# Kernel optimization log

Hardware: AMD Instinct MI355X
Metric: run time of the kernel (lower is better)

The kernel has to match this reference:

```python
import jax, jax.numpy as jnp
import numpy as np

B, M, D = 2048, 128, 5          # batch, max_atoms, max_degree
F_A, F_B, C = 62, 6, 128        # atom feats, bond feats, conv_width


def setup_inputs() -> dict:
    key = jax.random.key(0)
    k1, k2, k3, k4, k5 = jax.random.split(key, 5)
    atoms = jax.random.normal(k1, (B, M, F_A), dtype=jnp.float32)
    bonds = jax.random.uniform(k2, (B, M, D, F_B), dtype=jnp.float32)
    # edges in [-1, M-1]; -1 = no neighbour (padding)
    edges = jax.random.randint(k3, (B, M, D), 0, M + 1, dtype=jnp.int32) - 1
    fan = F_A + F_B
    scale = float(np.sqrt(2.0 / (fan + C)))
    W_inner = jax.random.normal(k4, (D, fan, C), dtype=jnp.float32) * scale
    b_inner = jnp.zeros((D, C), dtype=jnp.float32)
    W_self = jax.random.normal(k5, (fan, C), dtype=jnp.float32) * scale
    b_self = jnp.zeros((C,), dtype=jnp.float32)
    return {"atoms": atoms, "bonds": bonds, "edges": edges,
            "W_inner": W_inner, "b_inner": b_inner,
            "W_self": W_self, "b_self": b_self}


def reference(atoms, bonds, edges, W_inner, b_inner, W_self, b_self):
    # --- encode() of TiedGraphAutoencoder (encode_only=True) ---
    b = atoms.shape[0]
    # atom degree = number of non-(-1) entries per atom  (B, M)
    deg = jnp.sum((edges != -1).astype(jnp.float32), axis=-1)

    # neighbour_lookup: pad a zero atom at index 0, shift edges by +1,
    # batched gather -> (B, M, D, F_A)
    padded = jnp.pad(atoms, ((0, 0), (1, 0), (0, 0)))
    neigh = padded[jnp.arange(b)[:, None, None], edges + 1]

    summed_atoms = neigh.sum(axis=-2)          # (B, M, F_A)
    summed_bonds = bonds.sum(axis=-2)          # (B, M, F_B)
    summed_features = jnp.concatenate([summed_atoms, summed_bonds], axis=-1)

    # per-degree TimeDistributed Dense + relu, masked by (deg == d), summed
    h = jax.nn.relu(jnp.einsum('bmf,dfc->bmdc', summed_features, W_inner)
                    + b_inner)                 # (B, M, D, C)
    mask = (deg[..., None] == jnp.arange(D, dtype=jnp.float32)).astype(h.dtype)
    zni = jnp.einsum('bmdc,bmd->bmc', h, mask)  # (B, M, C)

    # self connection: dense on [atoms, summed_bonds]
    vxi = jnp.concatenate([atoms, summed_bonds], axis=-1)
    zxi = jax.nn.relu(vxi @ W_self + b_self)    # (B, M, C)

    return zni + zxi
```

## Files before the change

kernel.cpp:

```cpp
#include <hip/hip_runtime.h>

#define NB 2048
#define NM 128
#define ND 5
#define NFA 62
#define NFB 6
#define NFAN 68
#define NC 128
#define LDA 104
#define LDSF 72
#define CHUNK 32

typedef __bf16 bf16x8 __attribute__((ext_vector_type(8)));
typedef float floatx4 __attribute__((ext_vector_type(4)));

__device__ __forceinline__ unsigned short f2bf(float x) {
    unsigned u = __builtin_bit_cast(unsigned, x);
    u += 0x7FFFu + ((u >> 16) & 1u);
    return (unsigned short)(u >> 16);
}

__global__ __launch_bounds__(256) void tga_mfma(
    const float* __restrict__ atoms,
    const float* __restrict__ bonds,
    const int*   __restrict__ edges,
    const float* __restrict__ W_inner,
    const float* __restrict__ b_inner,
    const float* __restrict__ W_self,
    const float* __restrict__ b_self,
    float* __restrict__ out)
{
    __shared__ __align__(16) unsigned short s_A[NM * LDA];
    __shared__ __align__(16) unsigned short s_B[NC * LDA];
    __shared__ __align__(16) float s_sf[CHUNK * LDSF];
    __shared__ int s_list[NM];
    __shared__ int s_nlist;

    const int tid = threadIdx.x;
    const int b   = blockIdx.x;
    if (tid == 0) s_nlist = 0;

    const float* atoms_b = atoms + (size_t)b * (NM * NFA);
    const int*   edges_b = edges + (size_t)b * (NM * ND);
    const float* bonds_b = bonds + (size_t)b * (NM * ND * NFB);
    float*       out_b   = out   + (size_t)b * (NM * NC);

    for (int i = tid; i < NM * 31; i += 256) {
        int m = i / 31, p = i - m * 31;
        float2 v = *(const float2*)&atoms_b[m * NFA + 2 * p];
        unsigned pack = (unsigned)f2bf(v.x) | ((unsigned)f2bf(v.y) << 16);
        *(unsigned*)&s_A[m * LDA + 2 * p] = pack;
    }
    for (int i = tid; i < NM * 7; i += 256) {
        int m = i / 7, q = i - m * 7;
        *(unsigned long long*)&s_A[m * LDA + 68 + 4 * q] = 0ULL;
    }
    for (int i = tid; i < NFAN * NC; i += 256) {
        int f = i >> 7, c2 = i & 127;
        s_B[c2 * LDA + f] = f2bf(W_self[i]);
    }
    for (int i = tid; i < NC * 7; i += 256) {
        int c2 = i / 7, q = i - c2 * 7;
        *(unsigned long long*)&s_B[c2 * LDA + 68 + 4 * q] = 0ULL;
    }

    {
        const int m = tid >> 1, half = tid & 1;
        if (half == 0) {
            const int* e = edges_b + m * ND;
            int deg = 0;
            #pragma unroll
            for (int j = 0; j < ND; ++j) deg += (e[j] >= 0);
            if (deg < ND) {
                int slot = atomicAdd(&s_nlist, 1);
                s_list[slot] = m | (deg << 16);
            }
        } else {
            const float* bp = bonds_b + m * (ND * NFB);
            float sb[NFB] = {0.f, 0.f, 0.f, 0.f, 0.f, 0.f};
            #pragma unroll
            for (int p = 0; p < 15; ++p) {
                float2 v = *(const float2*)&bp[2 * p];
                sb[(2 * p) % NFB]     += v.x;
                sb[(2 * p + 1) % NFB] += v.y;
            }
            *(unsigned*)&s_A[m * LDA + 62] = (unsigned)f2bf(sb[0]) | ((unsigned)f2bf(sb[1]) << 16);
            *(unsigned*)&s_A[m * LDA + 64] = (unsigned)f2bf(sb[2]) | ((unsigned)f2bf(sb[3]) << 16);
            *(unsigned*)&s_A[m * LDA + 66] = (unsigned)f2bf(sb[4]) | ((unsigned)f2bf(sb[5]) << 16);
        }
    }
    __syncthreads();

    {
        const int lane = tid & 63;
        const int wave = tid >> 6;
        const int col  = lane & 15;
        const int quad = lane >> 4;
        const int m0   = wave * 32;

        float bias[8];
        #pragma unroll
        for (int nt = 0; nt < 8; ++nt) bias[nt] = b_self[nt * 16 + col];

        floatx4 acc[16];
        #pragma unroll
        for (int t = 0; t < 16; ++t) {
            floatx4 v; v[0] = v[1] = v[2] = v[3] = bias[t & 7];
            acc[t] = v;
        }

        #pragma unroll
        for (int k = 0; k < 3; ++k) {
            const int koff = k * 32 + quad * 8;
            bf16x8 a0 = *(const bf16x8*)&s_A[(m0 + col) * LDA + koff];
            bf16x8 a1 = *(const bf16x8*)&s_A[(m0 + 16 + col) * LDA + koff];
            #pragma unroll
            for (int nt = 0; nt < 8; ++nt) {
                bf16x8 bf = *(const bf16x8*)&s_B[(nt * 16 + col) * LDA + koff];
                acc[nt]     = __builtin_amdgcn_mfma_f32_16x16x32_bf16(a0, bf, acc[nt],     0, 0, 0);
                acc[8 + nt] = __builtin_amdgcn_mfma_f32_16x16x32_bf16(a1, bf, acc[8 + nt], 0, 0, 0);
            }
        }

        #pragma unroll
        for (int mt = 0; mt < 2; ++mt) {
            #pragma unroll
            for (int nt = 0; nt < 8; ++nt) {
                #pragma unroll
                for (int r = 0; r < 4; ++r) {
                    int m = m0 + mt * 16 + quad * 4 + r;
                    out_b[m * NC + nt * 16 + col] = fmaxf(acc[mt * 8 + nt][r], 0.0f);
                }
            }
        }
    }
    __syncthreads();

    const int nl = s_nlist;
    const int c  = tid & 127;
    const int rg = tid >> 7;

    for (int base = 0; base < nl; base += CHUNK) {
        if (tid < 2 * CHUNK) {
            const int r = tid >> 1, half = tid & 1;
            if (base + r < nl) {
                const int m = s_list[base + r] & 0xFFFF;
                const int* e = edges_b + m * ND;
                int ev[ND];
                #pragma unroll
                for (int j = 0; j < ND; ++j) ev[j] = e[j];

                if (half == 0) {
                    float v[32];
                    #pragma unroll
                    for (int j = 0; j < 32; ++j) v[j] = 0.f;
                    #pragma unroll
                    for (int j = 0; j < ND; ++j) {
                        if (ev[j] >= 0) {
                            const float* ap = atoms_b + ev[j] * NFA;
                            #pragma unroll
                            for (int p = 0; p < 16; ++p) {
                                float2 t = *(const float2*)&ap[2 * p];
                                v[2 * p] += t.x; v[2 * p + 1] += t.y;
                            }
                        }
                    }
                    #pragma unroll
                    for (int q = 0; q < 8; ++q)
                        *(float4*)&s_sf[r * LDSF + 4 * q] = make_float4(v[4*q], v[4*q+1], v[4*q+2], v[4*q+3]);
                } else {
                    float v[36];
                    #pragma unroll
                    for (int j = 0; j < 30; ++j) v[j] = 0.f;
                    #pragma unroll
                    for (int j = 0; j < ND; ++j) {
                        if (ev[j] >= 0) {
                            const float* ap = atoms_b + ev[j] * NFA;
                            #pragma unroll
                            for (int p = 0; p < 15; ++p) {
                                float2 t = *(const float2*)&ap[32 + 2 * p];
                                v[2 * p] += t.x; v[2 * p + 1] += t.y;
                            }
                        }
                    }
                    const float* bp = bonds_b + m * (ND * NFB);
                    float sb[NFB] = {0.f, 0.f, 0.f, 0.f, 0.f, 0.f};
                    #pragma unroll
                    for (int p = 0; p < 15; ++p) {
                        float2 t = *(const float2*)&bp[2 * p];
                        sb[(2 * p) % NFB]     += t.x;
                        sb[(2 * p + 1) % NFB] += t.y;
                    }
                    #pragma unroll
                    for (int j = 0; j < NFB; ++j) v[30 + j] = sb[j];
                    #pragma unroll
                    for (int q = 0; q < 9; ++q)
                        *(float4*)&s_sf[r * LDSF + 32 + 4 * q] = make_float4(v[4*q], v[4*q+1], v[4*q+2], v[4*q+3]);
                }
            }
        }
        __syncthreads();

        const int nrows = min(nl - base, CHUNK);
        for (int r = rg; r < nrows; r += 2) {
            const int packed = s_list[base + r];
            const int m = packed & 0xFFFF;
            const int d = packed >> 16;
            const float* Wd = W_inner + (size_t)d * (NFAN * NC) + c;
            float acc1 = b_inner[d * NC + c];
            #pragma unroll
            for (int q = 0; q < 17; ++q) {
                float4 v = *(const float4*)&s_sf[r * LDSF + 4 * q];
                acc1 += v.x * Wd[(4 * q) * NC] + v.y * Wd[(4 * q + 1) * NC]
                      + v.z * Wd[(4 * q + 2) * NC] + v.w * Wd[(4 * q + 3) * NC];
            }
            out_b[m * NC + c] += fmaxf(acc1, 0.0f);
        }
        __syncthreads();
    }
}

extern "C" void kernel_launch(void* const* d_in, const int* in_sizes, int n_in,
                              void* d_out, int out_size, void* d_ws, size_t ws_size,
                              hipStream_t stream) {
    const float* atoms   = (const float*)d_in[0];
    const float* bonds   = (const float*)d_in[1];
    const int*   edges   = (const int*)d_in[2];
    const float* W_inner = (const float*)d_in[3];
    const float* b_inner = (const float*)d_in[4];
    const float* W_self  = (const float*)d_in[5];
    const float* b_self  = (const float*)d_in[6];
    float* out = (float*)d_out;

    tga_mfma<<<NB, 256, 0, stream>>>(atoms, bonds, edges, W_inner, b_inner,
                                     W_self, b_self, out);
}
```

Before: 268.4 us.

## Pre-convert W_self to bf16 in a prep kernel and read it from global

```diff
diff --git a/kernel.cpp b/kernel.cpp
--- a/kernel.cpp
+++ b/kernel.cpp
@@ -7,9 +7,10 @@
 #define NFB 6
 #define NFAN 68
 #define NC 128
+#define KP 96
 #define LDA 104
 #define LDSF 72
-#define CHUNK 32
+#define CHUNK 16
 
 typedef __bf16 bf16x8 __attribute__((ext_vector_type(8)));
 typedef float floatx4 __attribute__((ext_vector_type(4)));
@@ -20,18 +21,27 @@
     return (unsigned short)(u >> 16);
 }
 
-__global__ __launch_bounds__(256) void tga_mfma(
+__global__ __launch_bounds__(256) void prep_w(const float* __restrict__ W_self,
+                                              unsigned short* __restrict__ wsb) {
+    const int i = blockIdx.x * 256 + threadIdx.x;
+    const int c = i / KP;
+    const int f = i - c * KP;
+    unsigned short v = 0;
+    if (f < NFAN) v = f2bf(W_self[f * NC + c]);
+    wsb[i] = v;
+}
+
+__global__ __launch_bounds__(256, 4) void tga_mfma(
     const float* __restrict__ atoms,
     const float* __restrict__ bonds,
     const int*   __restrict__ edges,
     const float* __restrict__ W_inner,
     const float* __restrict__ b_inner,
-    const float* __restrict__ W_self,
     const float* __restrict__ b_self,
+    const unsigned short* __restrict__ wsb,
     float* __restrict__ out)
 {
     __shared__ __align__(16) unsigned short s_A[NM * LDA];
-    __shared__ __align__(16) unsigned short s_B[NC * LDA];
     __shared__ __align__(16) float s_sf[CHUNK * LDSF];
     __shared__ int s_list[NM];
     __shared__ int s_nlist;
@@ -54,14 +64,6 @@
     for (int i = tid; i < NM * 7; i += 256) {
         int m = i / 7, q = i - m * 7;
         *(unsigned long long*)&s_A[m * LDA + 68 + 4 * q] = 0ULL;
-    }
-    for (int i = tid; i < NFAN * NC; i += 256) {
-        int f = i >> 7, c2 = i & 127;
-        s_B[c2 * LDA + f] = f2bf(W_self[i]);
-    }
-    for (int i = tid; i < NC * 7; i += 256) {
-        int c2 = i / 7, q = i - c2 * 7;
-        *(unsigned long long*)&s_B[c2 * LDA + 68 + 4 * q] = 0ULL;
     }
 
     {
@@ -98,16 +100,11 @@
         const int quad = lane >> 4;
         const int m0   = wave * 32;
 
-        float bias[8];
-        #pragma unroll
-        for (int nt = 0; nt < 8; ++nt) bias[nt] = b_self[nt * 16 + col];
-
         floatx4 acc[16];
         #pragma unroll
-        for (int t = 0; t < 16; ++t) {
-            floatx4 v; v[0] = v[1] = v[2] = v[3] = bias[t & 7];
-            acc[t] = v;
-        }
+        for (int t = 0; t < 16; ++t) { floatx4 z; z[0]=z[1]=z[2]=z[3]=0.f; acc[t] = z; }
+
+        const unsigned short* wb = wsb + col * KP + quad * 8;
 
         #pragma unroll
         for (int k = 0; k < 3; ++k) {
@@ -116,21 +113,20 @@
             bf16x8 a1 = *(const bf16x8*)&s_A[(m0 + 16 + col) * LDA + koff];
             #pragma unroll
             for (int nt = 0; nt < 8; ++nt) {
-                bf16x8 bf = *(const bf16x8*)&s_B[(nt * 16 + col) * LDA + koff];
+                bf16x8 bf = *(const bf16x8*)&wb[nt * 16 * KP + k * 32];
                 acc[nt]     = __builtin_amdgcn_mfma_f32_16x16x32_bf16(a0, bf, acc[nt],     0, 0, 0);
                 acc[8 + nt] = __builtin_amdgcn_mfma_f32_16x16x32_bf16(a1, bf, acc[8 + nt], 0, 0, 0);
             }
         }
 
         #pragma unroll
-        for (int mt = 0; mt < 2; ++mt) {
-            #pragma unroll
-            for (int nt = 0; nt < 8; ++nt) {
-                #pragma unroll
-                for (int r = 0; r < 4; ++r) {
-                    int m = m0 + mt * 16 + quad * 4 + r;
-                    out_b[m * NC + nt * 16 + col] = fmaxf(acc[mt * 8 + nt][r], 0.0f);
-                }
+        for (int nt = 0; nt < 8; ++nt) {
+            const float bias = b_self[nt * 16 + col];
+            #pragma unroll
+            for (int r = 0; r < 4; ++r) {
+                const int row0 = m0 + quad * 4 + r;
+                out_b[row0 * NC + nt * 16 + col]        = fmaxf(acc[nt][r]     + bias, 0.0f);
+                out_b[(row0 + 16) * NC + nt * 16 + col] = fmaxf(acc[8 + nt][r] + bias, 0.0f);
             }
         }
     }
@@ -231,7 +227,9 @@
     const float* W_self  = (const float*)d_in[5];
     const float* b_self  = (const float*)d_in[6];
     float* out = (float*)d_out;
-
+    unsigned short* wsb = (unsigned short*)d_ws;
+
+    prep_w<<<(NC * KP + 255) / 256, 256, 0, stream>>>(W_self, wsb);
     tga_mfma<<<NB, 256, 0, stream>>>(atoms, bonds, edges, W_inner, b_inner,
-                                     W_self, b_self, out);
-}
+                                     b_self, wsb, out);
+}
```

Measured after the change: 298.5 us. 11.2% more time.
